# Kernel optimization log

Measured on AMD Instinct MI355X. Metric: run time of the kernel, lower is better.

Reference implementation:

```python
import jax, jax.numpy as jnp
import numpy as np

# Video-DiT scale: d_model = H * D = 2048
B, S_T, S_C, H, D = 2, 2048, 1024, 16, 128


def setup_inputs() -> dict:
    key = jax.random.key(0)
    ks = jax.random.split(key, 6)
    f = lambda k, s: jax.random.normal(k, s, dtype=jnp.float32)
    return {
        "target_q": f(ks[0], (B, S_T, H, D)),
        "target_k": f(ks[1], (B, S_T, H, D)),
        "target_v": f(ks[2], (B, S_T, H, D)),
        "cond_k": f(ks[3], (B, S_C, H, D)),
        "cond_v": f(ks[4], (B, S_C, H, D)),
        "b_param": f(ks[5], (1,)),
    }


def reference(target_q, target_k, target_v, cond_k, cond_v, b_param):
    """Extended target self-attention over [target_k; cond_k] with a scalar
    logit bias b_param added only to the condition-key columns.
    Inputs BSHD; returns [B, S_t, H*D] (ready for output_proj)."""
    Bq, St, Hh, Dd = target_q.shape
    Sc = cond_k.shape[1]
    scale = Dd ** -0.5  # softmax_scale defaults to head_dim**-0.5

    k_ext = jnp.concatenate([target_k, cond_k], axis=1)  # [B, S_t+S_c, H, D]
    v_ext = jnp.concatenate([target_v, cond_v], axis=1)

    # [B, H, S_t, S_t+S_c]
    logits = jnp.einsum('bqhd,bkhd->bhqk', target_q, k_ext) * jnp.asarray(scale, target_q.dtype)
    # bias: 0 on target keys, b on cond keys
    bias = jnp.concatenate([
        jnp.zeros((St,), logits.dtype),
        jnp.broadcast_to(b_param.astype(logits.dtype), (Sc,)),
    ])
    logits = logits + bias[None, None, None, :]

    probs = jax.nn.softmax(logits, axis=-1)
    out = jnp.einsum('bhqk,bkhd->bqhd', probs, v_ext)  # [B, S_t, H, D]
    return out.reshape(Bq, St, Hh * Dd)
```

## Files before the change

kernel.cpp:

```cpp
#include <hip/hip_runtime.h>
#include <hip/hip_bf16.h>

typedef __attribute__((ext_vector_type(4))) float f32x4;
typedef __attribute__((ext_vector_type(16))) float f32x16;
typedef __attribute__((ext_vector_type(8))) short bf8;
typedef __attribute__((ext_vector_type(2))) int i32x2;

#define B_ 2
#define ST 2048
#define SC 1024
#define SK 3072
#define NH 16
#define DH 128
#define KVB 32
#define NT 96
#define TGT 64
#define SCALE 0.088388347648318447f

__device__ __forceinline__ unsigned short f2bf(float f) {
    union { __hip_bfloat16 b; unsigned short u; } c;
    c.b = __float2bfloat16(f);
    return c.u;
}

__device__ __forceinline__ i32x2 tr_read(unsigned a) {
    i32x2 d;
    asm volatile("ds_read_b64_tr_b16 %0, %1" : "=v"(d) : "v"(a));
    return d;
}

__device__ __forceinline__ unsigned cvtpk(float lo, float hi) {
    unsigned r;
    asm("v_cvt_pk_bf16_f32 %0, %1, %2" : "=v"(r) : "v"(lo), "v"(hi));
    return r;
}

__device__ __forceinline__ void swap32(unsigned &a, unsigned &b) {
    asm volatile("v_permlane32_swap_b32 %0, %1" : "+v"(a), "+v"(b));
}
__device__ __forceinline__ float xmax32(float x) {
    return fmaxf(x, __shfl_xor(x, 32));
}
__device__ __forceinline__ float xsum32(float x) {
    return x + __shfl_xor(x, 32);
}

__device__ __forceinline__ bf8 pack_bf8(f32x4 a, f32x4 b) {
    bf8 v;
    v[0]=(short)f2bf(a[0]); v[1]=(short)f2bf(a[1]);
    v[2]=(short)f2bf(a[2]); v[3]=(short)f2bf(a[3]);
    v[4]=(short)f2bf(b[0]); v[5]=(short)f2bf(b[1]);
    v[6]=(short)f2bf(b[2]); v[7]=(short)f2bf(b[3]);
    return v;
}

__device__ __forceinline__ bf8 mk_bf8(i32x2 a, i32x2 b) {
    union { i32x2 h[2]; bf8 v; } u;
    u.h[0] = a; u.h[1] = b;
    return u.v;
}
__device__ __forceinline__ bf8 mk_bf8w(unsigned w0, unsigned w1, unsigned w2, unsigned w3) {
    union { unsigned w[4]; bf8 v; } u;
    u.w[0] = w0; u.w[1] = w1; u.w[2] = w2; u.w[3] = w3;
    return u.v;
}

__global__ __launch_bounds__(256, 2)
void attn_fwd(const float* __restrict__ Q,
              const float* __restrict__ TK,
              const float* __restrict__ TV,
              const float* __restrict__ CK,
              const float* __restrict__ CV,
              const float* __restrict__ BP,
              float* __restrict__ OUT)
{
    __shared__ __align__(16) unsigned short Ks[2][KVB * DH];
    __shared__ __align__(16) unsigned short Vs[2][KVB * DH];

    const int tid = threadIdx.x;
    const int w   = tid >> 6;
    const int l   = tid & 63;
    const int r31 = l & 31;
    const int hi  = l >> 5;

    const int bid = blockIdx.x;
    const int xcd = bid & 7;
    const int sub = bid >> 3;
    const int bh  = xcd * 4 + (sub >> 4);
    const int qt  = sub & 15;
    const int bb  = bh >> 4;
    const int hh  = bh & 15;

    const float bias_c = BP[0];

    const int qrow = qt * 128 + w * 32 + r31;
    const float* qp = Q + (((size_t)bb * ST + qrow) * NH + hh) * DH;
    bf8 qf[8];
#pragma unroll
    for (int dk = 0; dk < 8; ++dk) {
        const f32x4 x0 = *(const f32x4*)(qp + dk * 16 + hi * 8);
        const f32x4 x1 = *(const f32x4*)(qp + dk * 16 + hi * 8 + 4);
        bf8 v;
        v[0]=(short)f2bf(x0[0]*SCALE); v[1]=(short)f2bf(x0[1]*SCALE);
        v[2]=(short)f2bf(x0[2]*SCALE); v[3]=(short)f2bf(x0[3]*SCALE);
        v[4]=(short)f2bf(x1[0]*SCALE); v[5]=(short)f2bf(x1[1]*SCALE);
        v[6]=(short)f2bf(x1[2]*SCALE); v[7]=(short)f2bf(x1[3]*SCALE);
        qf[dk] = v;
    }

    f32x16 oa[4];
#pragma unroll
    for (int dt = 0; dt < 4; ++dt)
#pragma unroll
        for (int e = 0; e < 16; ++e) oa[dt][e] = 0.f;
    float m_run = -1e30f, l_run = 0.f;

    f32x4 skr[2][2], svr[2][2];

    auto stage_load = [&](int t) {
        const int kv0 = t * KVB;
        const float *kb, *vb;
        if (kv0 < ST) {
            const size_t off = (((size_t)bb * ST + kv0) * NH + hh) * DH;
            kb = TK + off; vb = TV + off;
        } else {
            const size_t off = (((size_t)bb * SC + (kv0 - ST)) * NH + hh) * DH;
            kb = CK + off; vb = CV + off;
        }
#pragma unroll
        for (int i = 0; i < 2; ++i) {
            const int c = tid + (i << 8);
            const int krow = c >> 4;
            const int kcol = ((c & 15) ^ (krow & 7)) << 3;
            const float* kp = kb + (size_t)krow * (NH * DH) + kcol;
            skr[i][0] = *(const f32x4*)kp;
            skr[i][1] = *(const f32x4*)(kp + 4);
            const int vkv = (((c >> 8) & 1) << 4) | (((c >> 4) & 1) << 3)
                          | (((c >> 7) & 1) << 2) | ((c >> 1) & 3);
            const int vd  = (((c >> 5) & 3) << 5) | (((c >> 3) & 1) << 4)
                          | ((c & 1) << 3);
            const float* vp = vb + (size_t)vkv * (NH * DH) + vd;
            svr[i][0] = *(const f32x4*)vp;
            svr[i][1] = *(const f32x4*)(vp + 4);
        }
    };

    auto stage_write = [&](int buf) {
#pragma unroll
        for (int i = 0; i < 2; ++i) {
            const int c = tid + (i << 8);
            *(bf8*)((char*)Ks[buf] + c * 16) = pack_bf8(skr[i][0], skr[i][1]);
            *(bf8*)((char*)Vs[buf] + c * 16) = pack_bf8(svr[i][0], svr[i][1]);
        }
    };

    stage_load(0);
    stage_write(0);

    const unsigned vLane = (unsigned)(size_t)&Vs[0][0] + (unsigned)((l >> 4) * 128 + (l & 15) * 8);

    for (int t = 0; t < NT; ++t) {
        __syncthreads();
        if (t + 1 < NT) stage_load(t + 1);
        const int buf = t & 1;
        const float bias = (t >= TGT) ? bias_c : 0.f;

        f32x16 s0, s1;
#pragma unroll
        for (int e = 0; e < 16; ++e) { s0[e] = 0.f; s1[e] = 0.f; }
        __builtin_amdgcn_s_setprio(1);
#pragma unroll
        for (int dk = 0; dk < 8; dk += 2) {
            int o0 = r31 * 256 + (dk * 16 + hi * 8) * 2;
            o0 ^= (r31 & 7) << 4;
            const bf8 kf0 = *(const bf8*)((const char*)Ks[buf] + o0);
            s0 = __builtin_amdgcn_mfma_f32_32x32x16_bf16(kf0, qf[dk], s0, 0, 0, 0);
            int o1 = r31 * 256 + ((dk + 1) * 16 + hi * 8) * 2;
            o1 ^= (r31 & 7) << 4;
            const bf8 kf1 = *(const bf8*)((const char*)Ks[buf] + o1);
            s1 = __builtin_amdgcn_mfma_f32_32x32x16_bf16(kf1, qf[dk + 1], s1, 0, 0, 0);
        }
        __builtin_amdgcn_s_setprio(0);

        asm volatile("" ::: "memory");
        const unsigned vA = vLane + (unsigned)(buf << 13);
        i32x2 vt_[2][4][2];
#pragma unroll
        for (int ks = 0; ks < 2; ++ks) {
            const unsigned vk = vA + (unsigned)(ks << 12);
#pragma unroll
            for (int dt = 0; dt < 4; ++dt) {
                vt_[ks][dt][0] = tr_read(vk + dt * 512);
                vt_[ks][dt][1] = tr_read(vk + dt * 512 + 2048);
            }
        }

        float p[16];
#pragma unroll
        for (int e = 0; e < 16; ++e) p[e] = s0[e] + s1[e];

        float mx = p[0];
#pragma unroll
        for (int e = 1; e < 16; ++e) mx = fmaxf(mx, p[e]);
        mx = xmax32(mx) + bias;
        const int need = (mx > m_run + 8.f) ? 1 : 0;
        if (__any(need)) {
            const float mnew = fmaxf(m_run, mx);
            const float corr = __expf(m_run - mnew);
            m_run = mnew;
            l_run *= corr;
#pragma unroll
            for (int dt = 0; dt < 4; ++dt)
#pragma unroll
                for (int e = 0; e < 16; ++e) oa[dt][e] *= corr;
        }
        const float zb = bias - m_run;
        float rs = 0.f;
#pragma unroll
        for (int e = 0; e < 16; ++e) { p[e] = __expf(p[e] + zb); rs += p[e]; }
        l_run += xsum32(rs);

        unsigned a0 = cvtpk(p[0], p[1]),  b0 = cvtpk(p[4], p[5]);
        unsigned a1 = cvtpk(p[2], p[3]),  b1 = cvtpk(p[6], p[7]);
        swap32(a0, b0); swap32(a1, b1);
        const bf8 pf0 = mk_bf8w(a0, a1, b0, b1);
        unsigned a2 = cvtpk(p[8], p[9]),   b2 = cvtpk(p[12], p[13]);
        unsigned a3 = cvtpk(p[10], p[11]), b3 = cvtpk(p[14], p[15]);
        swap32(a2, b2); swap32(a3, b3);
        const bf8 pf1 = mk_bf8w(a2, a3, b2, b3);

        asm volatile("s_waitcnt lgkmcnt(0)");
        __builtin_amdgcn_sched_barrier(0);
        __builtin_amdgcn_s_setprio(1);
#pragma unroll
        for (int ks = 0; ks < 2; ++ks) {
            const bf8 pf = ks ? pf1 : pf0;
#pragma unroll
            for (int dt = 0; dt < 4; ++dt) {
                const bf8 vf = mk_bf8(vt_[ks][dt][0], vt_[ks][dt][1]);
                oa[dt] = __builtin_amdgcn_mfma_f32_32x32x16_bf16(vf, pf, oa[dt], 0, 0, 0);
            }
        }
        __builtin_amdgcn_s_setprio(0);

        if (t + 1 < NT) stage_write(buf ^ 1);
    }

    const float inv = 1.0f / l_run;
    float* op = OUT + ((size_t)(bb * ST + qrow)) * (NH * DH) + hh * DH;
#pragma unroll
    for (int dt = 0; dt < 4; ++dt)
#pragma unroll
        for (int rr = 0; rr < 4; ++rr) {
            f32x4 st;
            st[0] = oa[dt][rr * 4 + 0] * inv;
            st[1] = oa[dt][rr * 4 + 1] * inv;
            st[2] = oa[dt][rr * 4 + 2] * inv;
            st[3] = oa[dt][rr * 4 + 3] * inv;
            *(f32x4*)(op + dt * 32 + rr * 8 + hi * 4) = st;
        }
}

extern "C" void kernel_launch(void* const* d_in, const int* in_sizes, int n_in,
                              void* d_out, int out_size, void* d_ws, size_t ws_size,
                              hipStream_t stream) {
    const float* q  = (const float*)d_in[0];
    const float* tk = (const float*)d_in[1];
    const float* tv = (const float*)d_in[2];
    const float* ck = (const float*)d_in[3];
    const float* cv = (const float*)d_in[4];
    const float* bp = (const float*)d_in[5];
    float* out = (float*)d_out;
    attn_fwd<<<dim3((ST / 128) * B_ * NH), 256, 0, stream>>>(q, tk, tv, ck, cv, bp, out);
}
```

Baseline: 153.5 us.

## Process two KV tiles per barrier and switch softmax to exp2

```diff
diff --git a/kernel.cpp b/kernel.cpp
--- a/kernel.cpp
+++ b/kernel.cpp
@@ -14,8 +14,10 @@
 #define DH 128
 #define KVB 32
 #define NT 96
-#define TGT 64
+#define NP 48
+#define TGTP 32
 #define SCALE 0.088388347648318447f
+#define LOG2E 1.4426950408889634f
 
 __device__ __forceinline__ unsigned short f2bf(float f) {
     union { __hip_bfloat16 b; unsigned short u; } c;
@@ -74,8 +76,8 @@
               const float* __restrict__ BP,
               float* __restrict__ OUT)
 {
-    __shared__ __align__(16) unsigned short Ks[2][KVB * DH];
-    __shared__ __align__(16) unsigned short Vs[2][KVB * DH];
+    __shared__ __align__(16) unsigned short Ks[4][KVB * DH];
+    __shared__ __align__(16) unsigned short Vs[4][KVB * DH];
 
     const int tid = threadIdx.x;
     const int w   = tid >> 6;
@@ -91,20 +93,21 @@
     const int bb  = bh >> 4;
     const int hh  = bh & 15;
 
-    const float bias_c = BP[0];
+    const float biasl = BP[0] * LOG2E;
 
     const int qrow = qt * 128 + w * 32 + r31;
     const float* qp = Q + (((size_t)bb * ST + qrow) * NH + hh) * DH;
+    const float qsc = SCALE * LOG2E;
     bf8 qf[8];
 #pragma unroll
     for (int dk = 0; dk < 8; ++dk) {
         const f32x4 x0 = *(const f32x4*)(qp + dk * 16 + hi * 8);
         const f32x4 x1 = *(const f32x4*)(qp + dk * 16 + hi * 8 + 4);
         bf8 v;
-        v[0]=(short)f2bf(x0[0]*SCALE); v[1]=(short)f2bf(x0[1]*SCALE);
-        v[2]=(short)f2bf(x0[2]*SCALE); v[3]=(short)f2bf(x0[3]*SCALE);
-        v[4]=(short)f2bf(x1[0]*SCALE); v[5]=(short)f2bf(x1[1]*SCALE);
-        v[6]=(short)f2bf(x1[2]*SCALE); v[7]=(short)f2bf(x1[3]*SCALE);
+        v[0]=(short)f2bf(x0[0]*qsc); v[1]=(short)f2bf(x0[1]*qsc);
+        v[2]=(short)f2bf(x0[2]*qsc); v[3]=(short)f2bf(x0[3]*qsc);
+        v[4]=(short)f2bf(x1[0]*qsc); v[5]=(short)f2bf(x1[1]*qsc);
+        v[6]=(short)f2bf(x1[2]*qsc); v[7]=(short)f2bf(x1[3]*qsc);
         qf[dk] = v;
     }
 
@@ -115,135 +118,160 @@
         for (int e = 0; e < 16; ++e) oa[dt][e] = 0.f;
     float m_run = -1e30f, l_run = 0.f;
 
-    f32x4 skr[2][2], svr[2][2];
-
-    auto stage_load = [&](int t) {
-        const int kv0 = t * KVB;
-        const float *kb, *vb;
-        if (kv0 < ST) {
-            const size_t off = (((size_t)bb * ST + kv0) * NH + hh) * DH;
-            kb = TK + off; vb = TV + off;
-        } else {
-            const size_t off = (((size_t)bb * SC + (kv0 - ST)) * NH + hh) * DH;
-            kb = CK + off; vb = CV + off;
-        }
-#pragma unroll
-        for (int i = 0; i < 2; ++i) {
-            const int c = tid + (i << 8);
-            const int krow = c >> 4;
-            const int kcol = ((c & 15) ^ (krow & 7)) << 3;
-            const float* kp = kb + (size_t)krow * (NH * DH) + kcol;
-            skr[i][0] = *(const f32x4*)kp;
-            skr[i][1] = *(const f32x4*)(kp + 4);
-            const int vkv = (((c >> 8) & 1) << 4) | (((c >> 4) & 1) << 3)
-                          | (((c >> 7) & 1) << 2) | ((c >> 1) & 3);
-            const int vd  = (((c >> 5) & 3) << 5) | (((c >> 3) & 1) << 4)
-                          | ((c & 1) << 3);
-            const float* vp = vb + (size_t)vkv * (NH * DH) + vd;
-            svr[i][0] = *(const f32x4*)vp;
-            svr[i][1] = *(const f32x4*)(vp + 4);
+    int koff[2], voff[2];
+#pragma unroll
+    for (int i = 0; i < 2; ++i) {
+        const int c = tid + (i << 8);
+        const int krow = c >> 4;
+        const int kcol = ((c & 15) ^ (krow & 7)) << 3;
+        koff[i] = krow * (NH * DH) + kcol;
+        const int vkv = (((c >> 8) & 1) << 4) | (((c >> 4) & 1) << 3)
+                      | (((c >> 7) & 1) << 2) | ((c >> 1) & 3);
+        const int vd  = (((c >> 5) & 3) << 5) | (((c >> 3) & 1) << 4)
+                      | ((c & 1) << 3);
+        voff[i] = vkv * (NH * DH) + vd;
+    }
+
+    f32x4 skr[2][2][2], svr[2][2][2];
+
+    auto stage_load = [&](int p) {
+#pragma unroll
+        for (int ti = 0; ti < 2; ++ti) {
+            const int kv0 = (2 * p + ti) * KVB;
+            const float *kb, *vb;
+            if (kv0 < ST) {
+                const size_t off = (((size_t)bb * ST + kv0) * NH + hh) * DH;
+                kb = TK + off; vb = TV + off;
+            } else {
+                const size_t off = (((size_t)bb * SC + (kv0 - ST)) * NH + hh) * DH;
+                kb = CK + off; vb = CV + off;
+            }
+#pragma unroll
+            for (int i = 0; i < 2; ++i) {
+                const float* kp = kb + koff[i];
+                skr[ti][i][0] = *(const f32x4*)kp;
+                skr[ti][i][1] = *(const f32x4*)(kp + 4);
+                const float* vp = vb + voff[i];
+                svr[ti][i][0] = *(const f32x4*)vp;
+                svr[ti][i][1] = *(const f32x4*)(vp + 4);
+            }
         }
     };
 
-    auto stage_write = [&](int buf) {
-#pragma unroll
-        for (int i = 0; i < 2; ++i) {
-            const int c = tid + (i << 8);
-            *(bf8*)((char*)Ks[buf] + c * 16) = pack_bf8(skr[i][0], skr[i][1]);
-            *(bf8*)((char*)Vs[buf] + c * 16) = pack_bf8(svr[i][0], svr[i][1]);
+    auto stage_write = [&](int pb) {
+#pragma unroll
+        for (int ti = 0; ti < 2; ++ti) {
+            char* kd = (char*)Ks[2 * pb + ti];
+            char* vd = (char*)Vs[2 * pb + ti];
+#pragma unroll
+            for (int i = 0; i < 2; ++i) {
+                const int c = tid + (i << 8);
+                *(bf8*)(kd + c * 16) = pack_bf8(skr[ti][i][0], skr[ti][i][1]);
+                *(bf8*)(vd + c * 16) = pack_bf8(svr[ti][i][0], svr[ti][i][1]);
+            }
         }
     };
 
     stage_load(0);
     stage_write(0);
 
-    const unsigned vLane = (unsigned)(size_t)&Vs[0][0] + (unsigned)((l >> 4) * 128 + (l & 15) * 8);
-
-    for (int t = 0; t < NT; ++t) {
+    const unsigned vLane = (unsigned)(size_t)&Vs[0][0]
+                         + (unsigned)((l >> 4) * 128 + (l & 15) * 8);
+    const char* kBase = (const char*)Ks[0];
+
+    for (int tp = 0; tp < NP; ++tp) {
         __syncthreads();
-        if (t + 1 < NT) stage_load(t + 1);
-        const int buf = t & 1;
-        const float bias = (t >= TGT) ? bias_c : 0.f;
-
-        f32x16 s0, s1;
-#pragma unroll
-        for (int e = 0; e < 16; ++e) { s0[e] = 0.f; s1[e] = 0.f; }
-        __builtin_amdgcn_s_setprio(1);
-#pragma unroll
-        for (int dk = 0; dk < 8; dk += 2) {
-            int o0 = r31 * 256 + (dk * 16 + hi * 8) * 2;
-            o0 ^= (r31 & 7) << 4;
-            const bf8 kf0 = *(const bf8*)((const char*)Ks[buf] + o0);
-            s0 = __builtin_amdgcn_mfma_f32_32x32x16_bf16(kf0, qf[dk], s0, 0, 0, 0);
-            int o1 = r31 * 256 + ((dk + 1) * 16 + hi * 8) * 2;
-            o1 ^= (r31 & 7) << 4;
-            const bf8 kf1 = *(const bf8*)((const char*)Ks[buf] + o1);
-            s1 = __builtin_amdgcn_mfma_f32_32x32x16_bf16(kf1, qf[dk + 1], s1, 0, 0, 0);
+        if (tp + 1 < NP) stage_load(tp + 1);
+        const float bias = (tp >= TGTP) ? biasl : 0.f;
+
+#pragma unroll
+        for (int hf = 0; hf < 2; ++hf) {
+            const int buf = ((tp & 1) << 1) | hf;
+            const unsigned kOff = (unsigned)buf << 13;
+
+            f32x16 s0, s1;
+#pragma unroll
+            for (int e = 0; e < 16; ++e) { s0[e] = 0.f; s1[e] = 0.f; }
+            __builtin_amdgcn_s_setprio(1);
+#pragma unroll
+            for (int dk = 0; dk < 8; dk += 2) {
+                int o0 = r31 * 256 + (dk * 16 + hi * 8) * 2;
+                o0 ^= (r31 & 7) << 4;
+                const bf8 kf0 = *(const bf8*)(kBase + kOff + o0);
+                s0 = __builtin_amdgcn_mfma_f32_32x32x16_bf16(kf0, qf[dk], s0, 0, 0, 0);
+                int o1 = r31 * 256 + ((dk + 1) * 16 + hi * 8) * 2;
+                o1 ^= (r31 & 7) << 4;
+                const bf8 kf1 = *(const bf8*)(kBase + kOff + o1);
+                s1 = __builtin_amdgcn_mfma_f32_32x32x16_bf16(kf1, qf[dk + 1], s1, 0, 0, 0);
+            }
+            __builtin_amdgcn_s_setprio(0);
+
+            asm volatile("" ::: "memory");
+            const unsigned vA = vLane + ((unsigned)buf << 13);
+            i32x2 vt_[2][4][2];
+#pragma unroll
+            for (int ks = 0; ks < 2; ++ks) {
+                const unsigned vk = vA + (unsigned)(ks << 12);
+#pragma unroll
+                for (int dt = 0; dt < 4; ++dt) {
+                    vt_[ks][dt][0] = tr_read(vk + dt * 512);
+                    vt_[ks][dt][1] = tr_read(vk + dt * 512 + 2048);
+                }
+            }
+
+            float p[16];
+#pragma unroll
+            for (int e = 0; e < 16; ++e) p[e] = s0[e] + s1[e];
+
+            float mx = p[0];
+#pragma unroll
+            for (int e = 1; e < 16; ++e) mx = fmaxf(mx, p[e]);
+            mx = xmax32(mx) + bias;
+            const int need = (mx > m_run + 11.54f) ? 1 : 0;
+            if (__any(need)) {
+                const float mnew = fmaxf(m_run, mx);
+                const float corr = __builtin_amdgcn_exp2f(m_run - mnew);
+                m_run = mnew;
+                l_run *= corr;
+#pragma unroll
+                for (int dt = 0; dt < 4; ++dt)
+#pragma unroll
+                    for (int e = 0; e < 16; ++e) oa[dt][e] *= corr;
+            }
+            const float zb = bias - m_run;
+            float rs = 0.f;
+#pragma unroll
+            for (int e = 0; e < 16; ++e) {
+                p[e] = __builtin_amdgcn_exp2f(p[e] + zb);
+                rs += p[e];
+            }
+            l_run += xsum32(rs);
+
+            unsigned a0 = cvtpk(p[0], p[1]),  b0 = cvtpk(p[4], p[5]);
+            unsigned a1 = cvtpk(p[2], p[3]),  b1 = cvtpk(p[6], p[7]);
+            swap32(a0, b0); swap32(a1, b1);
+            const bf8 pf0 = mk_bf8w(a0, a1, b0, b1);
+            unsigned a2 = cvtpk(p[8], p[9]),   b2 = cvtpk(p[12], p[13]);
+            unsigned a3 = cvtpk(p[10], p[11]), b3 = cvtpk(p[14], p[15]);
+            swap32(a2, b2); swap32(a3, b3);
+            const bf8 pf1 = mk_bf8w(a2, a3, b2, b3);
+
+            asm volatile("s_waitcnt lgkmcnt(0)");
+            __builtin_amdgcn_sched_barrier(0);
+            __builtin_amdgcn_s_setprio(1);
+#pragma unroll
+            for (int ks = 0; ks < 2; ++ks) {
+                const bf8 pf = ks ? pf1 : pf0;
+#pragma unroll
+                for (int dt = 0; dt < 4; ++dt) {
+                    const bf8 vf = mk_bf8(vt_[ks][dt][0], vt_[ks][dt][1]);
+                    oa[dt] = __builtin_amdgcn_mfma_f32_32x32x16_bf16(vf, pf, oa[dt], 0, 0, 0);
+                }
+            }
+            __builtin_amdgcn_s_setprio(0);
         }
-        __builtin_amdgcn_s_setprio(0);
-
-        asm volatile("" ::: "memory");
-        const unsigned vA = vLane + (unsigned)(buf << 13);
-        i32x2 vt_[2][4][2];
-#pragma unroll
-        for (int ks = 0; ks < 2; ++ks) {
-            const unsigned vk = vA + (unsigned)(ks << 12);
-#pragma unroll
-            for (int dt = 0; dt < 4; ++dt) {
-                vt_[ks][dt][0] = tr_read(vk + dt * 512);
-                vt_[ks][dt][1] = tr_read(vk + dt * 512 + 2048);
-            }
-        }
-
-        float p[16];
-#pragma unroll
-        for (int e = 0; e < 16; ++e) p[e] = s0[e] + s1[e];
-
-        float mx = p[0];
-#pragma unroll
-        for (int e = 1; e < 16; ++e) mx = fmaxf(mx, p[e]);
-        mx = xmax32(mx) + bias;
-        const int need = (mx > m_run + 8.f) ? 1 : 0;
-        if (__any(need)) {
-            const float mnew = fmaxf(m_run, mx);
-            const float corr = __expf(m_run - mnew);
-            m_run = mnew;
-            l_run *= corr;
-#pragma unroll
-            for (int dt = 0; dt < 4; ++dt)
-#pragma unroll
-                for (int e = 0; e < 16; ++e) oa[dt][e] *= corr;
-        }
-        const float zb = bias - m_run;
-        float rs = 0.f;
-#pragma unroll
-        for (int e = 0; e < 16; ++e) { p[e] = __expf(p[e] + zb); rs += p[e]; }
-        l_run += xsum32(rs);
-
-        unsigned a0 = cvtpk(p[0], p[1]),  b0 = cvtpk(p[4], p[5]);
-        unsigned a1 = cvtpk(p[2], p[3]),  b1 = cvtpk(p[6], p[7]);
-        swap32(a0, b0); swap32(a1, b1);
-        const bf8 pf0 = mk_bf8w(a0, a1, b0, b1);
-        unsigned a2 = cvtpk(p[8], p[9]),   b2 = cvtpk(p[12], p[13]);
-        unsigned a3 = cvtpk(p[10], p[11]), b3 = cvtpk(p[14], p[15]);
-        swap32(a2, b2); swap32(a3, b3);
-        const bf8 pf1 = mk_bf8w(a2, a3, b2, b3);
-
-        asm volatile("s_waitcnt lgkmcnt(0)");
-        __builtin_amdgcn_sched_barrier(0);
-        __builtin_amdgcn_s_setprio(1);
-#pragma unroll
-        for (int ks = 0; ks < 2; ++ks) {
-            const bf8 pf = ks ? pf1 : pf0;
-#pragma unroll
-            for (int dt = 0; dt < 4; ++dt) {
-                const bf8 vf = mk_bf8(vt_[ks][dt][0], vt_[ks][dt][1]);
-                oa[dt] = __builtin_amdgcn_mfma_f32_32x32x16_bf16(vf, pf, oa[dt], 0, 0, 0);
-            }
-        }
-        __builtin_amdgcn_s_setprio(0);
-
-        if (t + 1 < NT) stage_write(buf ^ 1);
+
+        if (tp + 1 < NP) stage_write((tp + 1) & 1);
     }
 
     const float inv = 1.0f / l_run;
```

New measurement: 162.1 us. 1.06x slower.

## Split KV sequence across two wave groups per block with in-LDS softmax merge

Applied to the files above, without the earlier changes.

```diff
diff --git a/kernel.cpp b/kernel.cpp
--- a/kernel.cpp
+++ b/kernel.cpp
@@ -13,7 +13,7 @@
 #define NH 16
 #define DH 128
 #define KVB 32
-#define NT 96
+#define NTG 48
 #define TGT 64
 #define SCALE 0.088388347648318447f
 
@@ -65,7 +65,7 @@
     return u.v;
 }
 
-__global__ __launch_bounds__(256, 2)
+__global__ __launch_bounds__(512, 2)
 void attn_fwd(const float* __restrict__ Q,
               const float* __restrict__ TK,
               const float* __restrict__ TV,
@@ -74,14 +74,15 @@
               const float* __restrict__ BP,
               float* __restrict__ OUT)
 {
-    __shared__ __align__(16) unsigned short Ks[2][KVB * DH];
-    __shared__ __align__(16) unsigned short Vs[2][KVB * DH];
-
-    const int tid = threadIdx.x;
-    const int w   = tid >> 6;
-    const int l   = tid & 63;
-    const int r31 = l & 31;
-    const int hi  = l >> 5;
+    __shared__ __align__(16) char SM[66560];
+
+    const int tid  = threadIdx.x;
+    const int g    = tid >> 8;
+    const int t256 = tid & 255;
+    const int w4   = t256 >> 6;
+    const int l    = tid & 63;
+    const int r31  = l & 31;
+    const int hi   = l >> 5;
 
     const int bid = blockIdx.x;
     const int xcd = bid & 7;
@@ -93,7 +94,7 @@
 
     const float bias_c = BP[0];
 
-    const int qrow = qt * 128 + w * 32 + r31;
+    const int qrow = qt * 128 + w4 * 32 + r31;
     const float* qp = Q + (((size_t)bb * ST + qrow) * NH + hh) * DH;
     bf8 qf[8];
 #pragma unroll
@@ -118,7 +119,7 @@
     f32x4 skr[2][2], svr[2][2];
 
     auto stage_load = [&](int t) {
-        const int kv0 = t * KVB;
+        const int kv0 = (g * NTG + t) * KVB;
         const float *kb, *vb;
         if (kv0 < ST) {
             const size_t off = (((size_t)bb * ST + kv0) * NH + hh) * DH;
@@ -129,7 +130,7 @@
         }
 #pragma unroll
         for (int i = 0; i < 2; ++i) {
-            const int c = tid + (i << 8);
+            const int c = t256 + (i << 8);
             const int krow = c >> 4;
             const int kcol = ((c & 15) ^ (krow & 7)) << 3;
             const float* kp = kb + (size_t)krow * (NH * DH) + kcol;
@@ -146,24 +147,28 @@
     };
 
     auto stage_write = [&](int buf) {
+        char* kd = SM + (((g << 1) | buf) << 13);
+        char* vd = SM + 32768 + (((g << 1) | buf) << 13);
 #pragma unroll
         for (int i = 0; i < 2; ++i) {
-            const int c = tid + (i << 8);
-            *(bf8*)((char*)Ks[buf] + c * 16) = pack_bf8(skr[i][0], skr[i][1]);
-            *(bf8*)((char*)Vs[buf] + c * 16) = pack_bf8(svr[i][0], svr[i][1]);
+            const int c = t256 + (i << 8);
+            *(bf8*)(kd + c * 16) = pack_bf8(skr[i][0], skr[i][1]);
+            *(bf8*)(vd + c * 16) = pack_bf8(svr[i][0], svr[i][1]);
         }
     };
 
     stage_load(0);
     stage_write(0);
 
-    const unsigned vLane = (unsigned)(size_t)&Vs[0][0] + (unsigned)((l >> 4) * 128 + (l & 15) * 8);
-
-    for (int t = 0; t < NT; ++t) {
+    const unsigned smBase = (unsigned)(size_t)SM;
+    const unsigned vLaneOff = (unsigned)((l >> 4) * 128 + (l & 15) * 8);
+
+    for (int t = 0; t < NTG; ++t) {
         __syncthreads();
-        if (t + 1 < NT) stage_load(t + 1);
+        if (t + 1 < NTG) stage_load(t + 1);
         const int buf = t & 1;
-        const float bias = (t >= TGT) ? bias_c : 0.f;
+        const float bias = (g * NTG + t >= TGT) ? bias_c : 0.f;
+        const char* kB = SM + (((g << 1) | buf) << 13);
 
         f32x16 s0, s1;
 #pragma unroll
@@ -173,17 +178,17 @@
         for (int dk = 0; dk < 8; dk += 2) {
             int o0 = r31 * 256 + (dk * 16 + hi * 8) * 2;
             o0 ^= (r31 & 7) << 4;
-            const bf8 kf0 = *(const bf8*)((const char*)Ks[buf] + o0);
+            const bf8 kf0 = *(const bf8*)(kB + o0);
             s0 = __builtin_amdgcn_mfma_f32_32x32x16_bf16(kf0, qf[dk], s0, 0, 0, 0);
             int o1 = r31 * 256 + ((dk + 1) * 16 + hi * 8) * 2;
             o1 ^= (r31 & 7) << 4;
-            const bf8 kf1 = *(const bf8*)((const char*)Ks[buf] + o1);
+            const bf8 kf1 = *(const bf8*)(kB + o1);
             s1 = __builtin_amdgcn_mfma_f32_32x32x16_bf16(kf1, qf[dk + 1], s1, 0, 0, 0);
         }
         __builtin_amdgcn_s_setprio(0);
 
         asm volatile("" ::: "memory");
-        const unsigned vA = vLane + (unsigned)(buf << 13);
+        const unsigned vA = smBase + 32768u + (unsigned)((((g << 1) | buf)) << 13) + vLaneOff;
         i32x2 vt_[2][4][2];
 #pragma unroll
         for (int ks = 0; ks < 2; ++ks) {
@@ -243,22 +248,45 @@
         }
         __builtin_amdgcn_s_setprio(0);
 
-        if (t + 1 < NT) stage_write(buf ^ 1);
+        if (t + 1 < NTG) stage_write(buf ^ 1);
     }
 
-    const float inv = 1.0f / l_run;
-    float* op = OUT + ((size_t)(bb * ST + qrow)) * (NH * DH) + hh * DH;
-#pragma unroll
-    for (int dt = 0; dt < 4; ++dt)
-#pragma unroll
-        for (int rr = 0; rr < 4; ++rr) {
-            f32x4 st;
-            st[0] = oa[dt][rr * 4 + 0] * inv;
-            st[1] = oa[dt][rr * 4 + 1] * inv;
-            st[2] = oa[dt][rr * 4 + 2] * inv;
-            st[3] = oa[dt][rr * 4 + 3] * inv;
-            *(f32x4*)(op + dt * 32 + rr * 8 + hi * 4) = st;
-        }
+    __syncthreads();
+    float* xfer = (float*)(SM + w4 * 16384);
+    float* ml   = (float*)(SM + 65536);
+    if (g == 1) {
+#pragma unroll
+        for (int dt = 0; dt < 4; ++dt)
+#pragma unroll
+            for (int e = 0; e < 16; ++e)
+                xfer[(dt * 16 + e) * 64 + l] = oa[dt][e];
+        if (hi == 0) {
+            ml[(w4 * 32 + r31) * 2]     = m_run;
+            ml[(w4 * 32 + r31) * 2 + 1] = l_run;
+        }
+    }
+    __syncthreads();
+    if (g == 0) {
+        const float mb = ml[(w4 * 32 + r31) * 2];
+        const float lb = ml[(w4 * 32 + r31) * 2 + 1];
+        const float m  = fmaxf(m_run, mb);
+        const float ca = __expf(m_run - m);
+        const float cb = __expf(mb - m);
+        const float inv = 1.0f / (l_run * ca + lb * cb);
+        float* op = OUT + ((size_t)(bb * ST + qrow)) * (NH * DH) + hh * DH;
+#pragma unroll
+        for (int dt = 0; dt < 4; ++dt)
+#pragma unroll
+            for (int rr = 0; rr < 4; ++rr) {
+                f32x4 st;
+#pragma unroll
+                for (int j = 0; j < 4; ++j) {
+                    const float ob = xfer[(dt * 16 + rr * 4 + j) * 64 + l];
+                    st[j] = (oa[dt][rr * 4 + j] * ca + ob * cb) * inv;
+                }
+                *(f32x4*)(op + dt * 32 + rr * 8 + hi * 4) = st;
+            }
+    }
 }
 
 extern "C" void kernel_launch(void* const* d_in, const int* in_sizes, int n_in,
@@ -271,5 +299,5 @@
     const float* cv = (const float*)d_in[4];
     const float* bp = (const float*)d_in[5];
     float* out = (float*)d_out;
-    attn_fwd<<<dim3((ST / 128) * B_ * NH), 256, 0, stream>>>(q, tk, tv, ck, cv, bp, out);
-}
+    attn_fwd<<<dim3((ST / 128) * B_ * NH), 512, 0, stream>>>(q, tk, tv, ck, cv, bp, out);
+}
```

New measurement: 168.0 us. 9.5% more time.
